# Performance work log

Measured on AMD Instinct MI355X. Metric: run time of the kernel, lower is better.

Reference implementation:

```python
import jax, jax.numpy as jnp
import numpy as np
import math

B, N, S, H = 2, 4, 1024, 512
HEADS = 8
HEAD = H // HEADS
SCALE_BASE = 512  # xpos default scale_base
EPS = 1e-5        # GroupNorm eps


def _xpos_tables(seq_len, d):
    """Precompute xpos sin/cos/scale tables, duplicate-interleaved to width d."""
    half = d // 2
    scale_vec = (np.arange(0, d, 2) + 0.4 * d) / (1.4 * d)          # (half,)
    power = np.arange(seq_len)[:, None] / SCALE_BASE                # (S,1)
    scale = scale_vec[None, :] ** power                             # (S,half)
    inv_freq = 1.0 / (10000.0 ** (np.arange(half) / half))
    ang = np.arange(seq_len)[:, None] * inv_freq[None, :]           # (S,half)
    dup = lambda m: np.repeat(m, 2, axis=-1)                        # duplicate_interleave
    return (jnp.asarray(dup(np.sin(ang)), jnp.float32),
            jnp.asarray(dup(np.cos(ang)), jnp.float32),
            jnp.asarray(dup(scale), jnp.float32))


def _rot2(x):
    # rotate_every_two: (x0,x1,x2,x3,...) -> (-x1,x0,-x3,x2,...)
    x1 = x[..., ::2]
    x2 = x[..., 1::2]
    return jnp.stack([-x2, x1], axis=-1).reshape(x.shape)


def _decay_masks(seq_len, heads):
    # gammas from MultiScaleRetention.__init__; D[g,i,j] = gamma_g**(i-j) if i>=j else 0
    g = 1.0 - np.exp(np.linspace(math.log(1.0 / 32), math.log(1.0 / 512), heads))
    idx = np.arange(seq_len)
    diff = idx[:, None] - idx[None, :]
    D = np.where(diff >= 0, g[:, None, None] ** np.maximum(diff, 0), 0.0)
    return jnp.asarray(D, jnp.float32)


def setup_inputs():
    key = jax.random.key(0)
    ks = jax.random.split(key, 6)
    X = jax.random.normal(ks[0], (B, N, S, H), jnp.float32)
    W_Q = jax.random.normal(ks[1], (HEADS, H, HEAD), jnp.float32) / H
    W_K = jax.random.normal(ks[2], (HEADS, H, HEAD), jnp.float32) / H
    W_V = jax.random.normal(ks[3], (HEADS, H, HEAD), jnp.float32) / H
    W_G = jax.random.normal(ks[4], (H, H), jnp.float32) / H
    W_O = jax.random.normal(ks[5], (H, H), jnp.float32) / H
    gn_weight = jnp.ones((H,), jnp.float32)
    gn_bias = jnp.zeros((H,), jnp.float32)
    return {"X": X, "W_Q": W_Q, "W_K": W_K, "W_V": W_V,
            "W_G": W_G, "W_O": W_O, "gn_weight": gn_weight, "gn_bias": gn_bias}


def reference(X, W_Q, W_K, W_V, W_G, W_O, gn_weight, gn_bias):
    heads, _, head = W_Q.shape
    b, n, s, h = X.shape
    sin, cos, scale = _xpos_tables(s, head)   # each (s, head)
    D = _decay_masks(s, heads)                # (g, s, s)

    # per-head projections, all heads at once
    Q = jnp.einsum('bnsh,ghd->gbnsd', X, W_Q)
    K = jnp.einsum('bnsh,ghd->gbnsd', X, W_K)
    V = jnp.einsum('bnsh,ghd->gbnsd', X, W_V)
    # xpos rotary: Q upscaled, K downscaled
    Q = (Q * cos + _rot2(Q) * sin) * scale
    K = (K * cos + _rot2(K) * sin) / scale

    # decay-masked retention: (Q K^T * D) V per head
    scores = jnp.einsum('gbnsd,gbntd->gbnst', Q, K) * D[:, None, None]
    Y = jnp.einsum('gbnst,gbntd->gbnsd', scores, V)   # (g,b,n,s,head)

    # GroupNorm(heads groups over v_dim channels): normalize each head's channels
    mean = Y.mean(-1, keepdims=True)
    var = Y.var(-1, keepdims=True)
    Yn = (Y - mean) * jax.lax.rsqrt(var + EPS)
    Yn = Yn * gn_weight.reshape(heads, 1, 1, 1, head) + gn_bias.reshape(heads, 1, 1, 1, head)

    # concat heads on feature dim -> (b,n,s,v_dim)
    Ycat = jnp.moveaxis(Yn, 0, 3).reshape(b, n, s, heads * head)

    gate = X @ W_G
    gate = gate * jax.nn.sigmoid(gate)        # swish
    return (gate * Ycat) @ W_O
```

## Files before the change

kernel.cpp:

```cpp
#include <hip/hip_runtime.h>
#include <hip/hip_bf16.h>
#include <math.h>


typedef __attribute__((ext_vector_type(8))) short bf16x8;
typedef __attribute__((ext_vector_type(4))) float f32x4;

#define MFMA16(a, b, c) __builtin_amdgcn_mfma_f32_16x16x32_bf16(a, b, c, 0, 0, 0)
#define BAR() __builtin_amdgcn_s_barrier()
#define WAITV(n) asm volatile("s_waitcnt vmcnt(" #n ")" ::: "memory")
#define LGKM0() asm volatile("s_waitcnt lgkmcnt(0)" ::: "memory")

__device__ __forceinline__ unsigned short f2bf(float f) {
  union { float f; unsigned u; } x; x.f = f;
  unsigned r = x.u + 0x7FFFu + ((x.u >> 16) & 1u);
  return (unsigned short)(r >> 16);
}
__device__ __forceinline__ float bf2f(unsigned short b) {
  union { unsigned u; float f; } x; x.u = ((unsigned)b) << 16;
  return x.f;
}

__device__ __forceinline__ void gload_chunk(const unsigned short* gtile, size_t gstride,
                                            unsigned short* lds, int chunk, int lane) {
  int r = (chunk << 3) + (lane >> 3);
  int colel = ((lane & 7) ^ (lane >> 3)) << 3;
  const unsigned short* gp = gtile + (size_t)r * gstride + colel;
  __builtin_amdgcn_global_load_lds(
      (const __attribute__((address_space(1))) unsigned int*)gp,
      (__attribute__((address_space(3))) unsigned int*)((char*)lds + (chunk << 10)),
      16, 0, 0);
}

__device__ __forceinline__ bf16x8 frag64(const unsigned short* lds, int row, int colel) {
  return *(const bf16x8*)((const char*)lds + row * 128 + ((colel * 2) ^ ((row & 7) << 4)));
}


__global__ void k_prep(const float* __restrict__ X, const float* __restrict__ WQ,
                       const float* __restrict__ WK, const float* __restrict__ WV,
                       const float* __restrict__ WG, const float* __restrict__ WO,
                       unsigned short* __restrict__ Xb, unsigned short* __restrict__ Wcat,
                       unsigned short* __restrict__ WoT,
                       float2* __restrict__ qtab, float2* __restrict__ ktab) {
  int b = blockIdx.x, tid = threadIdx.x;
  if (b < 4096) {
    int idx = b * 256 + tid;
    float4 v = ((const float4*)X)[idx];
    ushort4 o;
    o.x = f2bf(v.x); o.y = f2bf(v.y); o.z = f2bf(v.z); o.w = f2bf(v.w);
    ((ushort4*)Xb)[idx] = o;
  } else if (b < 8192) {
    int idx = (b - 4096) * 256 + tid;
    int n = idx >> 9, k = idx & 511;
    float w;
    if (n < 1536) {
      const float* W = (n < 512) ? WQ : (n < 1024 ? WK : WV);
      int c = n & 511; int g = c >> 6, d = c & 63;
      w = W[((size_t)g * 512 + k) * 64 + d];
    } else {
      w = WG[(size_t)k * 512 + (n - 1536)];
    }
    Wcat[idx] = f2bf(w);
  } else if (b < 9216) {
    int idx = (b - 8192) * 256 + tid;
    int n = idx >> 9, k = idx & 511;
    WoT[idx] = f2bf(WO[(size_t)k * 512 + n]);
  } else {
    int idx = (b - 9216) * 256 + tid;
    int s = idx >> 5, i = idx & 31;
    double invf = pow(10000.0, -(double)i / 32.0);
    double ang = (double)s * invf;
    double sn = sin(ang), cs = cos(ang);
    double sv = (2.0 * i + 0.4 * 64.0) / (1.4 * 64.0);
    double sc = pow(sv, (double)s / 512.0);
    qtab[idx] = make_float2((float)(cs * sc), (float)(sn * sc));
    ktab[idx] = make_float2((float)(cs / sc), (float)(sn / sc));
  }
}


__launch_bounds__(512, 2)
__global__ void k_proj(const unsigned short* __restrict__ Xb, const unsigned short* __restrict__ Wt,
                       const float2* __restrict__ qtab, const float2* __restrict__ ktab,
                       unsigned short* __restrict__ Qb, unsigned short* __restrict__ Kb,
                       unsigned short* __restrict__ Vb, unsigned short* __restrict__ Gb) {
  __shared__ __attribute__((aligned(16))) unsigned short As[2][256 * 64];
  __shared__ __attribute__((aligned(16))) unsigned short Bs[2][256 * 64];
  const int tid = threadIdx.x, lane = tid & 63, wid = tid >> 6;
  const int wr = wid >> 2, wc = wid & 3;
  const int cb = blockIdx.x, rb = blockIdx.y;

  f32x4 acc[8][4] = {};
  const int kc = (lane >> 4) * 8;
  const unsigned short* Ag = Xb + (size_t)(rb * 256) * 512;
  const unsigned short* Bg = Wt + (size_t)(cb * 256) * 512;

#define PSTAGE(kt, buf)                                             \
  {                                                                 \
    _Pragma("unroll") for (int i = 0; i < 4; ++i) {                 \
      gload_chunk(Ag + (kt) * 64, 512, As[buf], wid * 4 + i, lane); \
      gload_chunk(Bg + (kt) * 64, 512, Bs[buf], wid * 4 + i, lane); \
    }                                                               \
  }

  PSTAGE(0, 0);
  for (int kt = 0; kt < 8; ++kt) {
    const int cur = kt & 1;
    if (kt < 7) {
      PSTAGE(kt + 1, cur ^ 1);
      WAITV(8);
    } else {
      WAITV(0);
    }
    BAR();
#pragma unroll
    for (int ks = 0; ks < 2; ++ks) {
      bf16x8 a[8], b[4];
#pragma unroll
      for (int mi = 0; mi < 8; ++mi) a[mi] = frag64(As[cur], wr * 128 + mi * 16 + (lane & 15), ks * 32 + kc);
#pragma unroll
      for (int ni = 0; ni < 4; ++ni) b[ni] = frag64(Bs[cur], wc * 64 + ni * 16 + (lane & 15), ks * 32 + kc);
#pragma unroll
      for (int mi = 0; mi < 8; ++mi)
#pragma unroll
        for (int ni = 0; ni < 4; ++ni)
          acc[mi][ni] = MFMA16(a[mi], b[ni], acc[mi][ni]);
    }
    LGKM0();
    BAR();
  }
#undef PSTAGE

  const int row0 = rb * 256 + wr * 128;
  const int colbase = cb * 256 + wc * 64;
  const int cls = cb >> 1;
  const float sgn = (lane & 1) ? 1.f : -1.f;

  if (cls <= 1) {
    const float2* tab = (cls == 0) ? qtab : ktab;
    unsigned short* dst = (cls == 0) ? Qb : Kb;
#pragma unroll
    for (int mi = 0; mi < 8; ++mi)
#pragma unroll
      for (int ni = 0; ni < 4; ++ni) {
        int d = ((colbase + ni * 16 + (lane & 15)) & 63);
        int i = d >> 1;
        int c = (colbase + ni * 16 + (lane & 15)) & 511;
#pragma unroll
        for (int r = 0; r < 4; ++r) {
          int row = row0 + mi * 16 + (lane >> 4) * 4 + r;
          int s = row & 1023;
          float v = acc[mi][ni][r];
          float p = __shfl_xor(v, 1);
          float2 t = tab[s * 32 + i];
          dst[(size_t)row * 512 + c] = f2bf(v * t.x + sgn * p * t.y);
        }
      }
  } else {
    unsigned short* dst = (cls == 2) ? Vb : Gb;
#pragma unroll
    for (int mi = 0; mi < 8; ++mi)
#pragma unroll
      for (int ni = 0; ni < 4; ++ni) {
        int c = (colbase + ni * 16 + (lane & 15)) & 511;
#pragma unroll
        for (int r = 0; r < 4; ++r) {
          int row = row0 + mi * 16 + (lane >> 4) * 4 + r;
          float v = acc[mi][ni][r];
          if (cls == 3) v = v / (1.f + __expf(-v));
          dst[(size_t)row * 512 + c] = f2bf(v);
        }
      }
  }
}


__launch_bounds__(256)
__global__ void k_ret(const unsigned short* __restrict__ Qb, const unsigned short* __restrict__ Kb,
                      const unsigned short* __restrict__ Vb, const unsigned short* __restrict__ Gb,
                      const float* __restrict__ gnw, const float* __restrict__ gnb,
                      unsigned short* __restrict__ Ab) {
  __shared__ __attribute__((aligned(16))) unsigned short Qs[128 * 64];
  __shared__ __attribute__((aligned(16))) unsigned short Ks[2][64 * 64];
  __shared__ __attribute__((aligned(16))) unsigned short Vs[2][64][72];
  __shared__ __attribute__((aligned(16))) unsigned short Ss[128][72];
  const int u = blockIdx.x;
  const int v = u & 255;
  const int hi = u >> 8;
  const int sraw = v & 7, g = (v >> 3) & 7;
  const int bn = (v >> 6) + (hi ? 4 : 0);
  const int sblk = hi ? 7 - sraw : sraw;
  const int tid = threadIdx.x, lane = tid & 63, w = tid >> 6;

  const float lg0 = logf(1.f / 32.f), lg1 = logf(1.f / 512.f);
  const float gam = 1.f - expf(lg0 + g * (lg1 - lg0) / 7.f);
  const float l2g = log2f(gam);

  const int s0 = sblk * 128;
  const size_t seqbase = (size_t)bn * 1024;
  const int kc = (lane >> 4) * 8;
  const int ntt = 2 * sblk + 2;

  float cf[16];
#pragma unroll
  for (int ti = 0; ti < 4; ++ti)
#pragma unroll
    for (int r = 0; r < 4; ++r)
      cf[ti * 4 + r] = exp2f(l2g * (float)(-(ti * 16 + (lane >> 4) * 4 + r)));
  const int sRow[2] = { w * 32 + (lane & 15), w * 32 + 16 + (lane & 15) };

  const int t0p = (tid >> 3) * 2;
  const int c0v = (tid & 7) * 8;
  const unsigned short* Vg = Vb + seqbase * 512 + g * 64 + c0v;

#define KSTAGE(t, buf)                                                        \
  {                                                                           \
    gload_chunk(Kb + (seqbase + (t) * 64) * 512 + g * 64, 512, Ks[buf], w * 2 + 0, lane); \
    gload_chunk(Kb + (seqbase + (t) * 64) * 512 + g * 64, 512, Ks[buf], w * 2 + 1, lane); \
  }
#define VLOAD(t, r0, r1)                                                      \
  {                                                                           \
    r0 = *(const bf16x8*)(Vg + (size_t)((t) * 64 + t0p) * 512);               \
    r1 = *(const bf16x8*)(Vg + (size_t)((t) * 64 + t0p + 1) * 512);           \
  }
#define VWRITE(buf, r0, r1)                                                   \
  {                                                                           \
    _Pragma("unroll") for (int j = 0; j < 8; ++j) {                           \
      int d = c0v + j;                                                        \
      ushort2 pp; pp.x = (unsigned short)r0[j]; pp.y = (unsigned short)r1[j]; \
      *(ushort2*)&Vs[buf][d][t0p ^ (d & 0x38)] = pp;                          \
    }                                                                         \
  }

  bf16x8 vA0, vA1, vB0, vB1;

  const unsigned short* Qg = Qb + (seqbase + s0) * 512 + g * 64;
#pragma unroll
  for (int i = 0; i < 4; ++i) gload_chunk(Qg, 512, Qs, w * 4 + i, lane);
  KSTAGE(0, 0);
  VLOAD(0, vA0, vA1);
  WAITV(0);
  VWRITE(0, vA0, vA1);
  KSTAGE(1, 1);
  VLOAD(1, vB0, vB1);
  LGKM0();
  BAR();

  bf16x8 qreg[2][2];
#pragma unroll
  for (int ks = 0; ks < 2; ++ks)
#pragma unroll
    for (int si = 0; si < 2; ++si)
      qreg[ks][si] = frag64(Qs, w * 32 + si * 16 + (lane & 15), ks * 32 + kc);

  f32x4 accY[2][4] = {};

  auto body = [&](int tt, int cur, bf16x8& w0, bf16x8& w1, bf16x8& l0, bf16x8& l1) {
    const int t0 = tt * 64;
    f32x4 accSt[4][2] = {};
#pragma unroll
    for (int ks = 0; ks < 2; ++ks) {
      bf16x8 kf[4];
#pragma unroll
      for (int ti = 0; ti < 4; ++ti) kf[ti] = frag64(Ks[cur], ti * 16 + (lane & 15), ks * 32 + kc);
#pragma unroll
      for (int ti = 0; ti < 4; ++ti)
#pragma unroll
        for (int si = 0; si < 2; ++si)
          accSt[ti][si] = MFMA16(kf[ti], qreg[ks][si], accSt[ti][si]);
    }

    float rf[2];
    rf[0] = exp2f(l2g * (float)(s0 + sRow[0] - t0));
    rf[1] = exp2f(l2g * (float)(s0 + sRow[1] - t0));
    if (tt >= 2 * sblk) {
#pragma unroll
      for (int ti = 0; ti < 4; ++ti)
#pragma unroll
        for (int si = 0; si < 2; ++si) {
          int tb = ti * 16 + (lane >> 4) * 4;
          ushort4 pk;
#pragma unroll
          for (int r = 0; r < 4; ++r) {
            int diff = (s0 + sRow[si]) - (t0 + tb + r);
            float dv = (diff >= 0) ? rf[si] * cf[ti * 4 + r] : 0.f;
            ((unsigned short*)&pk)[r] = f2bf(accSt[ti][si][r] * dv);
          }
          *(ushort4*)&Ss[sRow[si]][tb] = pk;
        }
    } else {
#pragma unroll
      for (int ti = 0; ti < 4; ++ti)
#pragma unroll
        for (int si = 0; si < 2; ++si) {
          int tb = ti * 16 + (lane >> 4) * 4;
          ushort4 pk;
#pragma unroll
          for (int r = 0; r < 4; ++r)
            ((unsigned short*)&pk)[r] = f2bf(accSt[ti][si][r] * rf[si] * cf[ti * 4 + r]);
          *(ushort4*)&Ss[sRow[si]][tb] = pk;
        }
    }

#pragma unroll
    for (int ks = 0; ks < 2; ++ks) {
      bf16x8 af[2], vf[4];
#pragma unroll
      for (int mi = 0; mi < 2; ++mi) af[mi] = *(const bf16x8*)&Ss[sRow[mi]][ks * 32 + kc];
#pragma unroll
      for (int ni = 0; ni < 4; ++ni) {
        int d = ni * 16 + (lane & 15);
        vf[ni] = *(const bf16x8*)&Vs[cur][d][(ks * 32 + kc) ^ (d & 0x38)];
      }
#pragma unroll
      for (int mi = 0; mi < 2; ++mi)
#pragma unroll
        for (int ni = 0; ni < 4; ++ni)
          accY[mi][ni] = MFMA16(af[mi], vf[ni], accY[mi][ni]);
    }

    LGKM0();
    BAR();
    if (tt + 1 < ntt) {
      WAITV(0);
      VWRITE(cur ^ 1, w0, w1);
      if (tt + 2 < ntt) {
        KSTAGE(tt + 2, cur);
        VLOAD(tt + 2, l0, l1);
      }
      LGKM0();
      BAR();
    }
  };

  for (int tt = 0; tt < ntt; tt += 2) {
    body(tt, 0, vB0, vB1, vA0, vA1);
    body(tt + 1, 1, vA0, vA1, vB0, vB1);
  }

  float gw[4], gbv[4];
#pragma unroll
  for (int ni = 0; ni < 4; ++ni) {
    int d = ni * 16 + (lane & 15);
    gw[ni] = gnw[g * 64 + d];
    gbv[ni] = gnb[g * 64 + d];
  }
#pragma unroll
  for (int mi = 0; mi < 2; ++mi)
#pragma unroll
    for (int r = 0; r < 4; ++r) {
      float sm = 0.f, sq = 0.f;
#pragma unroll
      for (int ni = 0; ni < 4; ++ni) { float v = accY[mi][ni][r]; sm += v; sq += v * v; }
#pragma unroll
      for (int off = 1; off < 16; off <<= 1) { sm += __shfl_xor(sm, off); sq += __shfl_xor(sq, off); }
      float mean = sm * (1.f / 64.f);
      float var = sq * (1.f / 64.f) - mean * mean;
      float rstd = rsqrtf(var + 1e-5f);
      int row = w * 32 + mi * 16 + (lane >> 4) * 4 + r;
      size_t grow = (seqbase + s0 + row) * 512 + g * 64;
#pragma unroll
      for (int ni = 0; ni < 4; ++ni) {
        int d = ni * 16 + (lane & 15);
        float vv = (accY[mi][ni][r] - mean) * rstd * gw[ni] + gbv[ni];
        float gate = bf2f(Gb[grow + d]);
        Ab[grow + d] = f2bf(vv * gate);
      }
    }
#undef KSTAGE
#undef VLOAD
#undef VWRITE
}


__launch_bounds__(256)
__global__ void k_out(const unsigned short* __restrict__ Ab, const unsigned short* __restrict__ Wt,
                      float* __restrict__ out) {
  __shared__ __attribute__((aligned(16))) unsigned short As[2][128 * 64];
  __shared__ __attribute__((aligned(16))) unsigned short Bs[2][64 * 64];
  const int tid = threadIdx.x, lane = tid & 63, wid = tid >> 6;
  const int wr = wid >> 1, wc = wid & 1;
  const int cb = blockIdx.x, rb = blockIdx.y;

  f32x4 acc[4][2] = {};
  const int kc = (lane >> 4) * 8;
  const unsigned short* Ag = Ab + (size_t)(rb * 128) * 512;
  const unsigned short* Bg = Wt + (size_t)(cb * 64) * 512;

#define OSTAGE(kt, buf)                                                  \
  {                                                                      \
    _Pragma("unroll") for (int i = 0; i < 4; ++i)                        \
        gload_chunk(Ag + (kt) * 64, 512, As[buf], wid * 4 + i, lane);    \
    _Pragma("unroll") for (int i = 0; i < 2; ++i)                        \
        gload_chunk(Bg + (kt) * 64, 512, Bs[buf], wid * 2 + i, lane);    \
  }

  OSTAGE(0, 0);
  for (int kt = 0; kt < 8; ++kt) {
    const int cur = kt & 1;
    if (kt < 7) {
      OSTAGE(kt + 1, cur ^ 1);
      WAITV(6);
    } else {
      WAITV(0);
    }
    BAR();
#pragma unroll
    for (int ks = 0; ks < 2; ++ks) {
      bf16x8 a[4], b[2];
#pragma unroll
      for (int mi = 0; mi < 4; ++mi) a[mi] = frag64(As[cur], wr * 64 + mi * 16 + (lane & 15), ks * 32 + kc);
#pragma unroll
      for (int ni = 0; ni < 2; ++ni) b[ni] = frag64(Bs[cur], wc * 32 + ni * 16 + (lane & 15), ks * 32 + kc);
#pragma unroll
      for (int mi = 0; mi < 4; ++mi)
#pragma unroll
        for (int ni = 0; ni < 2; ++ni)
          acc[mi][ni] = MFMA16(a[mi], b[ni], acc[mi][ni]);
    }
    LGKM0();
    BAR();
  }
#undef OSTAGE

  const int row0 = rb * 128 + wr * 64;
  const int col0 = cb * 64 + wc * 32;
#pragma unroll
  for (int mi = 0; mi < 4; ++mi)
#pragma unroll
    for (int ni = 0; ni < 2; ++ni) {
      int col = col0 + ni * 16 + (lane & 15);
#pragma unroll
      for (int r = 0; r < 4; ++r) {
        int row = row0 + mi * 16 + (lane >> 4) * 4 + r;
        out[(size_t)row * 512 + col] = acc[mi][ni][r];
      }
    }
}


extern "C" void kernel_launch(void* const* d_in, const int* in_sizes, int n_in,
                              void* d_out, int out_size, void* d_ws, size_t ws_size,
                              hipStream_t stream) {
  const float* X   = (const float*)d_in[0];
  const float* WQ  = (const float*)d_in[1];
  const float* WK  = (const float*)d_in[2];
  const float* WV  = (const float*)d_in[3];
  const float* WG  = (const float*)d_in[4];
  const float* WO  = (const float*)d_in[5];
  const float* gnw = (const float*)d_in[6];
  const float* gnb = (const float*)d_in[7];
  float* out = (float*)d_out;

  char* ws = (char*)d_ws;
  const size_t SZ_BUF = (size_t)8192 * 512 * 2;
  unsigned short* Xb   = (unsigned short*)(ws);
  unsigned short* Qb   = (unsigned short*)(ws + SZ_BUF);
  unsigned short* Kb   = (unsigned short*)(ws + 2 * SZ_BUF);
  unsigned short* Vb   = (unsigned short*)(ws + 3 * SZ_BUF);
  unsigned short* Gb   = (unsigned short*)(ws + 4 * SZ_BUF);
  unsigned short* Ab   = (unsigned short*)(ws + 5 * SZ_BUF);
  unsigned short* Wcat = (unsigned short*)(ws + 6 * SZ_BUF);
  unsigned short* WoT  = (unsigned short*)(ws + 6 * SZ_BUF + 2097152);
  float2* qtab = (float2*)(ws + 6 * SZ_BUF + 2097152 + 524288);
  float2* ktab = qtab + 32768;

  k_prep<<<9344, 256, 0, stream>>>(X, WQ, WK, WV, WG, WO, Xb, Wcat, WoT, qtab, ktab);
  k_proj<<<dim3(8, 32), 512, 0, stream>>>(Xb, Wcat, qtab, ktab, Qb, Kb, Vb, Gb);
  k_ret<<<512, 256, 0, stream>>>(Qb, Kb, Vb, Gb, gnw, gnb, Ab);
  k_out<<<dim3(8, 64), 256, 0, stream>>>(Ab, WoT, out);
}
```

Before: 158.1 us.

## Tile weight transposes via LDS, vectorize projection epilogue stores, use packed bf16 converts

The weight preparation now uses 64x64 LDS tiles, so both the reads and the writes of the transposed weight copies are coalesced, and the prep grid shrinks. The projection epilogue stages each accumulator tile through LDS. Each lane then applies rotary/swish on consecutive column pairs without shuffles and writes 16-byte vector stores instead of scattered 2-byte stores. Float-to-bf16 conversion switches to the packed v_cvt_pk_bf16_f32 instruction in several kernels, and the xpos tables are computed in float instead of double, which slightly changes precision.

```diff
diff --git a/kernel.cpp b/kernel.cpp
--- a/kernel.cpp
+++ b/kernel.cpp
@@ -10,6 +10,9 @@
 #define BAR() __builtin_amdgcn_s_barrier()
 #define WAITV(n) asm volatile("s_waitcnt vmcnt(" #n ")" ::: "memory")
 #define LGKM0() asm volatile("s_waitcnt lgkmcnt(0)" ::: "memory")
+#define CVTPK(a, b) ({ unsigned _r;                                   \
+  asm("v_cvt_pk_bf16_f32 %0, %1, %2" : "=v"(_r) : "v"(a), "v"(b));    \
+  _r; })
 
 __device__ __forceinline__ unsigned short f2bf(float f) {
   union { float f; unsigned u; } x; x.f = f;
@@ -47,35 +50,72 @@
   if (b < 4096) {
     int idx = b * 256 + tid;
     float4 v = ((const float4*)X)[idx];
-    ushort4 o;
-    o.x = f2bf(v.x); o.y = f2bf(v.y); o.z = f2bf(v.z); o.w = f2bf(v.w);
-    ((ushort4*)Xb)[idx] = o;
-  } else if (b < 8192) {
-    int idx = (b - 4096) * 256 + tid;
-    int n = idx >> 9, k = idx & 511;
-    float w;
-    if (n < 1536) {
-      const float* W = (n < 512) ? WQ : (n < 1024 ? WK : WV);
-      int c = n & 511; int g = c >> 6, d = c & 63;
-      w = W[((size_t)g * 512 + k) * 64 + d];
+    uint2 o;
+    o.x = CVTPK(v.x, v.y);
+    o.y = CVTPK(v.z, v.w);
+    ((uint2*)Xb)[idx] = o;
+    return;
+  }
+  if (b < 4416) {
+    __shared__ float Ls[64][68];
+    const float* src;
+    unsigned short* dst;
+    size_t src_ld, dst_rowbase, dst_colbase;
+    int b2;
+    if (b < 4288) {
+      b2 = b - 4096;
+      const float* W = (b2 < 64) ? WQ : (b2 < 128 ? WK : WV);
+      int cls = (b2 < 64) ? 0 : (b2 < 128 ? 1 : 2);
+      int gg = (b2 & 63) >> 3, kt = b2 & 7;
+      src = W + ((size_t)gg * 512 + kt * 64) * 64;
+      src_ld = 64;
+      dst = Wcat;
+      dst_rowbase = (size_t)cls * 512 + gg * 64;
+      dst_colbase = (size_t)kt * 64;
+    } else if (b < 4352) {
+      b2 = b - 4288;
+      int kt = b2 >> 3, nt = b2 & 7;
+      src = WG + (size_t)(kt * 64) * 512 + nt * 64;
+      src_ld = 512;
+      dst = Wcat;
+      dst_rowbase = 1536 + (size_t)nt * 64;
+      dst_colbase = (size_t)kt * 64;
     } else {
-      w = WG[(size_t)k * 512 + (n - 1536)];
-    }
-    Wcat[idx] = f2bf(w);
-  } else if (b < 9216) {
-    int idx = (b - 8192) * 256 + tid;
-    int n = idx >> 9, k = idx & 511;
-    WoT[idx] = f2bf(WO[(size_t)k * 512 + n]);
-  } else {
-    int idx = (b - 9216) * 256 + tid;
+      b2 = b - 4352;
+      int kt = b2 >> 3, nt = b2 & 7;
+      src = WO + (size_t)(kt * 64) * 512 + nt * 64;
+      src_ld = 512;
+      dst = WoT;
+      dst_rowbase = (size_t)nt * 64;
+      dst_colbase = (size_t)kt * 64;
+    }
+#pragma unroll
+    for (int i = 0; i < 4; ++i) {
+      int e = i * 256 + tid;
+      int r = e >> 4, c4 = e & 15;
+      float4 v = *(const float4*)(src + (size_t)r * src_ld + c4 * 4);
+      *(float4*)&Ls[r][c4 * 4] = v;
+    }
+    __syncthreads();
+    int d = tid >> 2, kp = (tid & 3) * 16;
+    unsigned short tmp[16];
+#pragma unroll
+    for (int k = 0; k < 16; ++k) tmp[k] = f2bf(Ls[kp + k][d]);
+    size_t orow = (dst_rowbase + d) * 512 + dst_colbase + kp;
+    *(bf16x8*)(dst + orow) = *(bf16x8*)&tmp[0];
+    *(bf16x8*)(dst + orow + 8) = *(bf16x8*)&tmp[8];
+    return;
+  }
+  {
+    int idx = (b - 4416) * 256 + tid;
     int s = idx >> 5, i = idx & 31;
-    double invf = pow(10000.0, -(double)i / 32.0);
-    double ang = (double)s * invf;
-    double sn = sin(ang), cs = cos(ang);
-    double sv = (2.0 * i + 0.4 * 64.0) / (1.4 * 64.0);
-    double sc = pow(sv, (double)s / 512.0);
-    qtab[idx] = make_float2((float)(cs * sc), (float)(sn * sc));
-    ktab[idx] = make_float2((float)(cs / sc), (float)(sn / sc));
+    float invf = exp2f(-(float)i * (13.2877123795f / 32.0f));
+    float ang = (float)s * invf;
+    float sn = sinf(ang), cs = cosf(ang);
+    float sv = (2.f * i + 25.6f) / 89.6f;
+    float sc = exp2f(log2f(sv) * (float)s * (1.f / 512.f));
+    qtab[idx] = make_float2(cs * sc, sn * sc);
+    ktab[idx] = make_float2(cs / sc, sn / sc);
   }
 }
 
@@ -132,46 +172,53 @@
   }
 #undef PSTAGE
 
+  float* patch = (float*)As + wid * (16 * 68);
+  const int rr = lane >> 2;
+  const int c0 = (lane & 3) * 16;
   const int row0 = rb * 256 + wr * 128;
-  const int colbase = cb * 256 + wc * 64;
+  const int colc = (cb & 1) * 256 + wc * 64;
   const int cls = cb >> 1;
-  const float sgn = (lane & 1) ? 1.f : -1.f;
-
-  if (cls <= 1) {
-    const float2* tab = (cls == 0) ? qtab : ktab;
-    unsigned short* dst = (cls == 0) ? Qb : Kb;
-#pragma unroll
-    for (int mi = 0; mi < 8; ++mi)
-#pragma unroll
-      for (int ni = 0; ni < 4; ++ni) {
-        int d = ((colbase + ni * 16 + (lane & 15)) & 63);
-        int i = d >> 1;
-        int c = (colbase + ni * 16 + (lane & 15)) & 511;
-#pragma unroll
-        for (int r = 0; r < 4; ++r) {
-          int row = row0 + mi * 16 + (lane >> 4) * 4 + r;
-          int s = row & 1023;
-          float v = acc[mi][ni][r];
-          float p = __shfl_xor(v, 1);
-          float2 t = tab[s * 32 + i];
-          dst[(size_t)row * 512 + c] = f2bf(v * t.x + sgn * p * t.y);
-        }
+  const int i0 = c0 >> 1;
+
+#pragma unroll
+  for (int mi = 0; mi < 8; ++mi) {
+#pragma unroll
+    for (int ni = 0; ni < 4; ++ni)
+#pragma unroll
+      for (int r = 0; r < 4; ++r)
+        patch[((lane >> 4) * 4 + r) * 68 + ni * 16 + (lane & 15)] = acc[mi][ni][r];
+    float v[16];
+#pragma unroll
+    for (int q = 0; q < 4; ++q) {
+      float4 t = *(float4*)&patch[rr * 68 + c0 + q * 4];
+      v[q * 4 + 0] = t.x; v[q * 4 + 1] = t.y; v[q * 4 + 2] = t.z; v[q * 4 + 3] = t.w;
+    }
+    int grow = row0 + mi * 16 + rr;
+    int s = grow & 1023;
+    unsigned out[8];
+    if (cls <= 1) {
+      const float2* tab = (cls == 0) ? qtab : ktab;
+#pragma unroll
+      for (int p = 0; p < 8; ++p) {
+        float2 t = tab[s * 32 + i0 + p];
+        float e = v[2 * p], o = v[2 * p + 1];
+        out[p] = CVTPK(e * t.x - o * t.y, o * t.x + e * t.y);
       }
-  } else {
-    unsigned short* dst = (cls == 2) ? Vb : Gb;
-#pragma unroll
-    for (int mi = 0; mi < 8; ++mi)
-#pragma unroll
-      for (int ni = 0; ni < 4; ++ni) {
-        int c = (colbase + ni * 16 + (lane & 15)) & 511;
-#pragma unroll
-        for (int r = 0; r < 4; ++r) {
-          int row = row0 + mi * 16 + (lane >> 4) * 4 + r;
-          float v = acc[mi][ni][r];
-          if (cls == 3) v = v / (1.f + __expf(-v));
-          dst[(size_t)row * 512 + c] = f2bf(v);
-        }
+    } else if (cls == 2) {
+#pragma unroll
+      for (int p = 0; p < 8; ++p) out[p] = CVTPK(v[2 * p], v[2 * p + 1]);
+    } else {
+#pragma unroll
+      for (int p = 0; p < 8; ++p) {
+        float e = v[2 * p], o = v[2 * p + 1];
+        e = e / (1.f + __expf(-e));
+        o = o / (1.f + __expf(-o));
+        out[p] = CVTPK(e, o);
       }
+    }
+    unsigned short* dst = (cls == 0) ? Qb : (cls == 1) ? Kb : (cls == 2) ? Vb : Gb;
+    *(uint4*)(dst + (size_t)grow * 512 + colc + c0) = *(uint4*)&out[0];
+    *(uint4*)(dst + (size_t)grow * 512 + colc + c0 + 8) = *(uint4*)&out[4];
   }
 }
 
@@ -280,14 +327,15 @@
 #pragma unroll
         for (int si = 0; si < 2; ++si) {
           int tb = ti * 16 + (lane >> 4) * 4;
-          ushort4 pk;
+          float p[4];
 #pragma unroll
           for (int r = 0; r < 4; ++r) {
             int diff = (s0 + sRow[si]) - (t0 + tb + r);
             float dv = (diff >= 0) ? rf[si] * cf[ti * 4 + r] : 0.f;
-            ((unsigned short*)&pk)[r] = f2bf(accSt[ti][si][r] * dv);
+            p[r] = accSt[ti][si][r] * dv;
           }
-          *(ushort4*)&Ss[sRow[si]][tb] = pk;
+          uint2 pk; pk.x = CVTPK(p[0], p[1]); pk.y = CVTPK(p[2], p[3]);
+          *(uint2*)&Ss[sRow[si]][tb] = pk;
         }
     } else {
 #pragma unroll
@@ -295,11 +343,12 @@
 #pragma unroll
         for (int si = 0; si < 2; ++si) {
           int tb = ti * 16 + (lane >> 4) * 4;
-          ushort4 pk;
-#pragma unroll
-          for (int r = 0; r < 4; ++r)
-            ((unsigned short*)&pk)[r] = f2bf(accSt[ti][si][r] * rf[si] * cf[ti * 4 + r]);
-          *(ushort4*)&Ss[sRow[si]][tb] = pk;
+          uint2 pk;
+          pk.x = CVTPK(accSt[ti][si][0] * rf[si] * cf[ti * 4 + 0],
+                       accSt[ti][si][1] * rf[si] * cf[ti * 4 + 1]);
+          pk.y = CVTPK(accSt[ti][si][2] * rf[si] * cf[ti * 4 + 2],
+                       accSt[ti][si][3] * rf[si] * cf[ti * 4 + 3]);
+          *(uint2*)&Ss[sRow[si]][tb] = pk;
         }
     }
 
@@ -352,7 +401,7 @@
     for (int r = 0; r < 4; ++r) {
       float sm = 0.f, sq = 0.f;
 #pragma unroll
-      for (int ni = 0; ni < 4; ++ni) { float v = accY[mi][ni][r]; sm += v; sq += v * v; }
+      for (int ni = 0; ni < 4; ++ni) { float vv = accY[mi][ni][r]; sm += vv; sq += vv * vv; }
 #pragma unroll
       for (int off = 1; off < 16; off <<= 1) { sm += __shfl_xor(sm, off); sq += __shfl_xor(sq, off); }
       float mean = sm * (1.f / 64.f);
@@ -466,7 +515,7 @@
   float2* qtab = (float2*)(ws + 6 * SZ_BUF + 2097152 + 524288);
   float2* ktab = qtab + 32768;
 
-  k_prep<<<9344, 256, 0, stream>>>(X, WQ, WK, WV, WG, WO, Xb, Wcat, WoT, qtab, ktab);
+  k_prep<<<4544, 256, 0, stream>>>(X, WQ, WK, WV, WG, WO, Xb, Wcat, WoT, qtab, ktab);
   k_proj<<<dim3(8, 32), 512, 0, stream>>>(Xb, Wcat, qtab, ktab, Qb, Kb, Vb, Gb);
   k_ret<<<512, 256, 0, stream>>>(Qb, Kb, Vb, Gb, gnw, gnb, Ab);
   k_out<<<dim3(8, 64), 256, 0, stream>>>(Ab, WoT, out);
```

After: 149.8 us. -5.2%, faster.
